# Kernel optimization log

Measured on AMD Instinct MI355X. Metric: run time of the kernel, lower is better.

Reference implementation:

```python
import jax, jax.numpy as jnp
import numpy as np

EPS = 1e-16


def setup_inputs() -> dict:
    key = jax.random.key(0)
    ks = jax.random.split(key, 7)
    B, N, C = 4096, 2048, 128  # batch of heads, memory rows, memory cols
    k = jax.random.normal(ks[0], (B, C), dtype=jnp.float32)
    beta = jax.random.normal(ks[1], (B, 1), dtype=jnp.float32)
    g = jax.random.normal(ks[2], (B, 1), dtype=jnp.float32)
    s = jax.random.normal(ks[3], (B, 3), dtype=jnp.float32)
    gamma = jax.random.normal(ks[4], (B, 1), dtype=jnp.float32)
    w_prev = jax.random.uniform(ks[5], (B, N), dtype=jnp.float32)
    w_prev = w_prev / jnp.sum(w_prev, axis=1, keepdims=True)  # valid weighting
    M = jax.random.normal(ks[6], (N, C), dtype=jnp.float32)  # memory matrix
    return {"k": k, "beta": beta, "g": g, "s": s, "gamma": gamma,
            "w_prev": w_prev, "M": M}


def reference(k, beta, g, s, gamma, w_prev, M):
    # head activations
    beta = jax.nn.softplus(beta)            # [B,1] key strength > 0
    g = jax.nn.sigmoid(g)                   # [B,1] interpolation gate
    s = jax.nn.softmax(s, axis=-1)          # [B,3] shift distribution
    gamma = 1.0 + jax.nn.softplus(gamma)    # [B,1] sharpening >= 1

    # content addressing: cosine similarity k vs memory rows
    k_norm = jnp.linalg.norm(k, axis=-1, keepdims=True)          # [B,1]
    m_norm = jnp.linalg.norm(M, axis=-1, keepdims=True)          # [N,1]
    sim = jnp.einsum('bc,nc->bn', k, M) / (k_norm * m_norm.T + EPS)  # [B,N]
    w_c = jax.nn.softmax(beta * sim, axis=-1)                    # [B,N]

    # interpolation with previous weighting
    w_g = g * w_c + (1.0 - g) * w_prev                           # [B,N]

    # circular convolution with 3-tap shift kernel (shifts -1, 0, +1)
    w_tilde = (s[:, 0:1] * jnp.roll(w_g, 1, axis=1)
               + s[:, 1:2] * w_g
               + s[:, 2:3] * jnp.roll(w_g, -1, axis=1))          # [B,N]

    # sharpening
    w_sharp = w_tilde ** gamma
    w = w_sharp / (jnp.sum(w_sharp, axis=1, keepdims=True) + EPS)
    return w
```

## Files before the change

### kernel.cpp

```cpp
#include <hip/hip_runtime.h>
#include <math.h>

#define NN 2048
#define CC 128
#define EPSF 1e-16f

typedef __attribute__((ext_vector_type(8))) short bf16x8;
typedef __attribute__((ext_vector_type(4))) float f32x4;

__device__ __forceinline__ float softplusf(float x) {
  return fmaxf(x, 0.0f) + log1pf(__expf(-fabsf(x)));
}
__device__ __forceinline__ float wave_sum(float v) {
#pragma unroll
  for (int o = 32; o; o >>= 1) v += __shfl_xor(v, o, 64);
  return v;
}

union U8 { uint u[4]; bf16x8 v; };

__device__ __forceinline__ void split8(float4 a, float4 b, bf16x8& hi,
                                       bf16x8& lo, float& sq) {
  float f[8] = {a.x, a.y, a.z, a.w, b.x, b.y, b.z, b.w};
  U8 H, L;
#pragma unroll
  for (int i = 0; i < 4; ++i) {
    float f0 = f[2 * i], f1 = f[2 * i + 1];
    sq += f0 * f0;
    sq += f1 * f1;
    uint u0 = __float_as_uint(f0), u1 = __float_as_uint(f1);
    uint m0 = u0 & 0xffff0000u, m1 = u1 & 0xffff0000u;
    float r0 = f0 - __uint_as_float(m0);
    float r1 = f1 - __uint_as_float(m1);
    H.u[i] = (u0 >> 16) | m1;
    L.u[i] = (__float_as_uint(r0) >> 16) | (__float_as_uint(r1) & 0xffff0000u);
  }
  hi = H.v;
  lo = L.v;
}

__device__ __forceinline__ void gl2lds16(const void* gsrc, void* ldst) {
  __builtin_amdgcn_global_load_lds(
      (const __attribute__((address_space(1))) void*)gsrc,
      (__attribute__((address_space(3))) void*)ldst, 16, 0, 0);
}

__global__ __launch_bounds__(256) void ntm_prep_kernel(
    const float* __restrict__ kptr, const float* __restrict__ beta_,
    const float* __restrict__ g_, const float* __restrict__ s_,
    const float* __restrict__ gamma_, const float* __restrict__ M,
    bf16x8* __restrict__ Mhf, bf16x8* __restrict__ Mlf,
    bf16x8* __restrict__ Khf, bf16x8* __restrict__ Klf,
    float* __restrict__ imn, float* __restrict__ zb, float* __restrict__ gvv,
    float* __restrict__ gmv, float* __restrict__ s0a, float* __restrict__ s1a,
    float* __restrict__ s2a) {
  const int bid = blockIdx.x;
  const int t = threadIdx.x;
  if (bid < 96) {
    const int lane = t & 63;
    const int wv = t >> 6;
    const int l15 = lane & 15;
    const int lg = lane >> 4;
    const bool isM = bid < 32;
    const int grp = (isM ? bid : bid - 32) * 4 + wv;
    const int nrow = isM ? ((grp >> 3) * 128 + 8 * l15 + (grp & 7))
                         : (grp * 16 + l15);
    const float* src = (isM ? M : kptr) + nrow * CC + lg * 8;
    bf16x8* dh = (isM ? Mhf : Khf) + (grp * 4) * 64 + lane;
    bf16x8* dl = (isM ? Mlf : Klf) + (grp * 4) * 64 + lane;
    float sq = 0.f;
#pragma unroll
    for (int ks = 0; ks < 4; ++ks) {
      float4 a0 = *(const float4*)(src + ks * 32);
      float4 a1 = *(const float4*)(src + ks * 32 + 4);
      bf16x8 h, l;
      split8(a0, a1, h, l, sq);
      dh[ks * 64] = h;
      dl[ks * 64] = l;
    }
    sq += __shfl_xor(sq, 16, 64);
    sq += __shfl_xor(sq, 32, 64);
    if (lg == 0) {
      if (isM) {
        imn[nrow] = 1.0f / sqrtf(sq);
      } else {
        zb[nrow] = softplusf(beta_[nrow]) / sqrtf(sq);
      }
    }
  } else {
    const int r = (bid - 96) * 256 + t;
    gvv[r] = 1.0f / (1.0f + __expf(-g_[r]));
    gmv[r] = 1.0f + softplusf(gamma_[r]);
    float sh0 = s_[3 * r], sh1 = s_[3 * r + 1], sh2 = s_[3 * r + 2];
    float shm = fmaxf(sh0, fmaxf(sh1, sh2));
    float e0 = __expf(sh0 - shm), e1 = __expf(sh1 - shm), e2 = __expf(sh2 - shm);
    float sden = 1.0f / (e0 + e1 + e2);
    s0a[r] = e0 * sden;
    s1a[r] = e1 * sden;
    s2a[r] = e2 * sden;
  }
}

__global__ __launch_bounds__(1024) void ntm_main_kernel(
    const float* __restrict__ w_prev, const bf16x8* __restrict__ Mhf,
    const bf16x8* __restrict__ Mlf, const bf16x8* __restrict__ Khf,
    const bf16x8* __restrict__ Klf, const float* __restrict__ imn,
    const float* __restrict__ zb, const float* __restrict__ gvv,
    const float* __restrict__ gmv, const float* __restrict__ s0a,
    const float* __restrict__ s1a, const float* __restrict__ s2a,
    float* __restrict__ out) {
  __shared__ __align__(16) char smem[131072];
  char* Areg = smem;
  float (*eQ)[2048] = (float(*)[2048])smem;

  const int t = threadIdx.x;
  const int lane = t & 63;
  const int w = __builtin_amdgcn_readfirstlane(t >> 6);
  const int l15 = lane & 15;
  const int lg = lane >> 4;
  const int bg = blockIdx.x;
  const int b0 = bg * 16;

  if (w == 0) {
#pragma unroll
    for (int ks = 0; ks < 4; ++ks) {
      gl2lds16(&Khf[(bg * 4 + ks) * 64 + lane], Areg + (ks * 2 + 0) * 1024);
      gl2lds16(&Klf[(bg * 4 + ks) * 64 + lane], Areg + (ks * 2 + 1) * 1024);
    }
  }
  char* myB = smem + 8192 + w * 4096;
  const int gw = 8 * w;
#define STAGEB(c)                                                          \
  {                                                                        \
    const int ks_ = (c) >> 3, tt_ = (c)&7;                                 \
    gl2lds16(&Mhf[((gw + tt_) * 4 + ks_) * 64 + lane],                     \
             myB + ((c)&1) * 2048);                                        \
    gl2lds16(&Mlf[((gw + tt_) * 4 + ks_) * 64 + lane],                     \
             myB + ((c)&1) * 2048 + 1024);                                 \
  }
  STAGEB(0);
  STAGEB(1);
  __syncthreads();

  f32x4 accT[8];
#pragma unroll
  for (int tt = 0; tt < 8; ++tt) accT[tt] = (f32x4){0.f, 0.f, 0.f, 0.f};

  bf16x8 ah, al;
#pragma unroll
  for (int c = 0; c < 32; ++c) {
    if ((c & 7) == 0) {
      const int ks_ = c >> 3;
      ah = *(const bf16x8*)(Areg + (ks_ * 2 + 0) * 1024 + lane * 16);
      al = *(const bf16x8*)(Areg + (ks_ * 2 + 1) * 1024 + lane * 16);
    }
    if (c == 31) {
      asm volatile("s_waitcnt vmcnt(0)" ::: "memory");
    } else {
      asm volatile("s_waitcnt vmcnt(2)" ::: "memory");
    }
    bf16x8 bh = *(const bf16x8*)(myB + (c & 1) * 2048 + lane * 16);
    bf16x8 bl = *(const bf16x8*)(myB + (c & 1) * 2048 + 1024 + lane * 16);
    asm volatile("s_waitcnt lgkmcnt(0)" ::: "memory");
    if (c + 2 < 32) STAGEB(c + 2);
    const int tt = c & 7;
    accT[tt] = __builtin_amdgcn_mfma_f32_16x16x32_bf16(ah, bh, accT[tt], 0, 0, 0);
    accT[tt] = __builtin_amdgcn_mfma_f32_16x16x32_bf16(al, bh, accT[tt], 0, 0, 0);
    accT[tt] = __builtin_amdgcn_mfma_f32_16x16x32_bf16(ah, bl, accT[tt], 0, 0, 0);
  }
#undef STAGEB

  const int ncol0 = 128 * w + 8 * l15;
  const float4 i0 = *(const float4*)&imn[ncol0];
  const float4 i1 = *(const float4*)&imn[ncol0 + 4];
  float imn_t[8] = {i0.x, i0.y, i0.z, i0.w, i1.x, i1.y, i1.z, i1.w};
#pragma unroll
  for (int q = 0; q < 4; ++q) {
    const float zbv = zb[b0 + lg * 4 + q];
#pragma unroll
    for (int tt = 0; tt < 8; ++tt) {
      accT[tt][q] = __expf(accT[tt][q] * imn_t[tt] * zbv);
    }
  }

  __syncthreads();

#pragma unroll
  for (int q = 0; q < 4; ++q) {
    *(float4*)&eQ[lg * 4 + q][ncol0] =
        (float4){accT[0][q], accT[1][q], accT[2][q], accT[3][q]};
    *(float4*)&eQ[lg * 4 + q][ncol0 + 4] =
        (float4){accT[4][q], accT[5][q], accT[6][q], accT[7][q]};
  }
  __syncthreads();

  float4 v[8];
#pragma unroll
  for (int b = 0; b < 8; ++b)
    v[b] = *(const float4*)&eQ[w][256 * b + 4 * lane];

  const int row = b0 + w;
  const int lanem1 = (lane + 63) & 63;
  const int lanep1 = (lane + 1) & 63;

  float lsum = 0.f;
#pragma unroll
  for (int b = 0; b < 8; ++b)
    lsum += (v[b].x + v[b].y) + (v[b].z + v[b].w);
  const float tot = wave_sum(lsum);

  const float gv = gvv[row];
  const float ge = gv / tot;
  const float om = 1.0f - gv;
  const float sh0 = s0a[row], sh1 = s1a[row], sh2 = s2a[row];
  const float gammav = gmv[row];

  const float4* w_prev4 = (const float4*)w_prev;
  const size_t rf4 = (size_t)row * (NN / 4) + lane;
#pragma unroll
  for (int b = 0; b < 8; ++b) {
    float4 w4 = w_prev4[rf4 + 64 * b];
    v[b].x = ge * v[b].x + om * w4.x;
    v[b].y = ge * v[b].y + om * w4.y;
    v[b].z = ge * v[b].z + om * w4.z;
    v[b].w = ge * v[b].w + om * w4.w;
  }

  float pm[8], np[8];
#pragma unroll
  for (int b = 0; b < 8; ++b) {
    pm[b] = __shfl(v[b].w, lanem1, 64);
    np[b] = __shfl(v[b].x, lanep1, 64);
  }
  float sp = 0.f;
#pragma unroll
  for (int b = 0; b < 8; ++b) {
    const float pv0 = (lane == 0) ? pm[(b + 7) & 7] : pm[b];
    const float nx3 = (lane == 63) ? np[(b + 1) & 7] : np[b];
    const float w0 = v[b].x, w1 = v[b].y, w2 = v[b].z, w3 = v[b].w;
    float t0 = sh0 * pv0 + sh1 * w0 + sh2 * w1;
    float t1 = sh0 * w0 + sh1 * w1 + sh2 * w2;
    float t2 = sh0 * w1 + sh1 * w2 + sh2 * w3;
    float t3 = sh0 * w2 + sh1 * w3 + sh2 * nx3;
    float p0 = __expf(gammav * __logf(t0));
    float p1 = __expf(gammav * __logf(t1));
    float p2 = __expf(gammav * __logf(t2));
    float p3 = __expf(gammav * __logf(t3));
    v[b].x = p0;
    v[b].y = p1;
    v[b].z = p2;
    v[b].w = p3;
    sp += (p0 + p1) + (p2 + p3);
  }
  const float spt = wave_sum(sp);
  const float pinv = 1.0f / (spt + EPSF);

  float4* out4 = (float4*)out;
#pragma unroll
  for (int b = 0; b < 8; ++b) {
    float4 o;
    o.x = v[b].x * pinv;
    o.y = v[b].y * pinv;
    o.z = v[b].z * pinv;
    o.w = v[b].w * pinv;
    out4[rf4 + 64 * b] = o;
  }
}

__global__ __launch_bounds__(1024) void ntm_main_fallback(
    const float* __restrict__ kptr, const float* __restrict__ beta_,
    const float* __restrict__ g_, const float* __restrict__ s_,
    const float* __restrict__ gamma_, const float* __restrict__ w_prev,
    const float* __restrict__ Mptr, float* __restrict__ out) {
  __shared__ float red[16][16];
  __shared__ float edges[16][16][2];
  const int t = threadIdx.x;
  const int lane = t & 63;
  const int w = __builtin_amdgcn_readfirstlane(t >> 6);
  const int l15 = lane & 15;
  const int lg = lane >> 4;
  const int b0 = blockIdx.x * 16;

  const float* kr = kptr + (b0 + l15) * CC + lg * 8;
  bf16x8 ah[4], al[4];
  float ksq = 0.f;
#pragma unroll
  for (int ks = 0; ks < 4; ++ks) {
    float4 a0 = *(const float4*)(kr + ks * 32);
    float4 a1 = *(const float4*)(kr + ks * 32 + 4);
    split8(a0, a1, ah[ks], al[ks], ksq);
  }
  ksq += __shfl_xor(ksq, 16, 64);
  ksq += __shfl_xor(ksq, 32, 64);
  const float ikn_own = 1.0f / sqrtf(ksq);

  f32x4 accT[8];
  float imn[8];
#pragma unroll
  for (int tt = 0; tt < 8; ++tt) {
    const int n0t = 128 * w + 16 * tt;
    const float* mr = Mptr + (size_t)(n0t + l15) * CC + lg * 8;
    f32x4 acc = {0.f, 0.f, 0.f, 0.f};
    float msq = 0.f;
#pragma unroll
    for (int ks = 0; ks < 4; ++ks) {
      float4 m0 = *(const float4*)(mr + ks * 32);
      float4 m1 = *(const float4*)(mr + ks * 32 + 4);
      bf16x8 bh, bl;
      split8(m0, m1, bh, bl, msq);
      acc = __builtin_amdgcn_mfma_f32_16x16x32_bf16(ah[ks], bh, acc, 0, 0, 0);
      acc = __builtin_amdgcn_mfma_f32_16x16x32_bf16(al[ks], bh, acc, 0, 0, 0);
      acc = __builtin_amdgcn_mfma_f32_16x16x32_bf16(ah[ks], bl, acc, 0, 0, 0);
    }
    msq += __shfl_xor(msq, 16, 64);
    msq += __shfl_xor(msq, 32, 64);
    imn[tt] = 1.0f / sqrtf(msq);
    accT[tt] = acc;
  }

#pragma unroll
  for (int q = 0; q < 4; ++q) {
    const int rr = lg * 4 + q;
    const float zb = softplusf(beta_[b0 + rr]) * __shfl(ikn_own, rr, 64);
    float rs = 0.f;
#pragma unroll
    for (int tt = 0; tt < 8; ++tt) {
      float e = __expf(accT[tt][q] * imn[tt] * zb);
      accT[tt][q] = e;
      rs += e;
    }
    rs += __shfl_xor(rs, 1, 64);
    rs += __shfl_xor(rs, 2, 64);
    rs += __shfl_xor(rs, 4, 64);
    rs += __shfl_xor(rs, 8, 64);
    if (l15 == 0) red[rr][w] = rs;
  }
  __syncthreads();

#pragma unroll
  for (int q = 0; q < 4; ++q) {
    const int rr = lg * 4 + q;
    float4 p0 = *(const float4*)&red[rr][0];
    float4 p1 = *(const float4*)&red[rr][4];
    float4 p2 = *(const float4*)&red[rr][8];
    float4 p3 = *(const float4*)&red[rr][12];
    float tot = (p0.x + p0.y + p0.z + p0.w) + (p1.x + p1.y + p1.z + p1.w) +
                (p2.x + p2.y + p2.z + p2.w) + (p3.x + p3.y + p3.z + p3.w);
    const float gv = 1.0f / (1.0f + __expf(-g_[b0 + rr]));
    const float ge = gv / tot;
    const float om = 1.0f - gv;
    const size_t rbase = (size_t)(b0 + rr) * NN + 128 * w + l15;
#pragma unroll
    for (int tt = 0; tt < 8; ++tt) {
      float wpv = w_prev[rbase + 16 * tt];
      accT[tt][q] = ge * accT[tt][q] + om * wpv;
    }
    if (l15 == 0) edges[rr][w][0] = accT[0][q];
    if (l15 == 15) edges[rr][w][1] = accT[7][q];
  }
  __syncthreads();

  const int tm = (lane & 48) | ((lane + 15) & 15);
  const int tp = (lane & 48) | ((lane + 1) & 15);
#pragma unroll
  for (int q = 0; q < 4; ++q) {
    const int rr = lg * 4 + q;
    float sh0 = s_[3 * (b0 + rr)];
    float sh1 = s_[3 * (b0 + rr) + 1];
    float sh2 = s_[3 * (b0 + rr) + 2];
    float shm = fmaxf(sh0, fmaxf(sh1, sh2));
    float e0 = __expf(sh0 - shm), e1 = __expf(sh1 - shm), e2 = __expf(sh2 - shm);
    float sden = 1.0f / (e0 + e1 + e2);
    sh0 = e0 * sden; sh1 = e1 * sden; sh2 = e2 * sden;
    const float gammav = 1.0f + softplusf(gamma_[b0 + rr]);
    const float eL = edges[rr][(w + 15) & 15][1];
    const float eR = edges[rr][(w + 1) & 15][0];
    float sm[8], sp[8];
#pragma unroll
    for (int tt = 0; tt < 8; ++tt) {
      sm[tt] = __shfl(accT[tt][q], tm, 64);
      sp[tt] = __shfl(accT[tt][q], tp, 64);
    }
    float rs = 0.f;
#pragma unroll
    for (int tt = 0; tt < 8; ++tt) {
      float pv = (l15 == 0) ? ((tt == 0) ? eL : sm[tt - 1]) : sm[tt];
      float nx = (l15 == 15) ? ((tt == 7) ? eR : sp[tt + 1]) : sp[tt];
      float wt = sh0 * pv + sh1 * accT[tt][q] + sh2 * nx;
      float p = __expf(gammav * __logf(wt));
      accT[tt][q] = p;
      rs += p;
    }
    rs += __shfl_xor(rs, 1, 64);
    rs += __shfl_xor(rs, 2, 64);
    rs += __shfl_xor(rs, 4, 64);
    rs += __shfl_xor(rs, 8, 64);
    if (l15 == 0) red[rr][w] = rs;
  }
  __syncthreads();

#pragma unroll
  for (int q = 0; q < 4; ++q) {
    const int rr = lg * 4 + q;
    float4 p0 = *(const float4*)&red[rr][0];
    float4 p1 = *(const float4*)&red[rr][4];
    float4 p2 = *(const float4*)&red[rr][8];
    float4 p3 = *(const float4*)&red[rr][12];
    float tot = (p0.x + p0.y + p0.z + p0.w) + (p1.x + p1.y + p1.z + p1.w) +
                (p2.x + p2.y + p2.z + p2.w) + (p3.x + p3.y + p3.z + p3.w);
    const float pinv = 1.0f / (tot + EPSF);
    const size_t rbase = (size_t)(b0 + rr) * NN + 128 * w + l15;
#pragma unroll
    for (int tt = 0; tt < 8; ++tt) {
      out[rbase + 16 * tt] = accT[tt][q] * pinv;
    }
  }
}

extern "C" void kernel_launch(void* const* d_in, const int* in_sizes, int n_in,
                              void* d_out, int out_size, void* d_ws, size_t ws_size,
                              hipStream_t stream) {
  const float* k = (const float*)d_in[0];
  const float* beta = (const float*)d_in[1];
  const float* g = (const float*)d_in[2];
  const float* s = (const float*)d_in[3];
  const float* gamma = (const float*)d_in[4];
  const float* w_prev = (const float*)d_in[5];
  const float* M = (const float*)d_in[6];
  float* out = (float*)d_out;

  char* ws = (char*)d_ws;
  bf16x8* Mhf = (bf16x8*)(ws + 0);
  bf16x8* Mlf = (bf16x8*)(ws + 524288);
  bf16x8* Khf = (bf16x8*)(ws + 1048576);
  bf16x8* Klf = (bf16x8*)(ws + 2097152);
  float* imn = (float*)(ws + 3145728);
  float* zb = imn + 2048;
  float* gvv = zb + 4096;
  float* gmv = gvv + 4096;
  float* s0a = gmv + 4096;
  float* s1a = s0a + 4096;
  float* s2a = s1a + 4096;
  const size_t need = 3145728 + 2048 * 4 + 6 * 4096 * 4;

  if (ws_size >= need) {
    ntm_prep_kernel<<<112, 256, 0, stream>>>(k, beta, g, s, gamma, M, Mhf, Mlf,
                                             Khf, Klf, imn, zb, gvv, gmv, s0a,
                                             s1a, s2a);
    ntm_main_kernel<<<256, 1024, 0, stream>>>(w_prev, Mhf, Mlf, Khf, Klf, imn,
                                              zb, gvv, gmv, s0a, s1a, s2a, out);
  } else {
    ntm_main_fallback<<<256, 1024, 0, stream>>>(k, beta, g, s, gamma, w_prev,
                                                M, out);
  }
}
```

Measured before the change: 39.25 us.

## Prescale M and k by norms in prep, triple-buffer M tiles, raise MFMA priority

```diff
diff --git a/kernel.cpp b/kernel.cpp
--- a/kernel.cpp
+++ b/kernel.cpp
@@ -19,15 +19,11 @@
 
 union U8 { uint u[4]; bf16x8 v; };
 
-__device__ __forceinline__ void split8(float4 a, float4 b, bf16x8& hi,
-                                       bf16x8& lo, float& sq) {
-  float f[8] = {a.x, a.y, a.z, a.w, b.x, b.y, b.z, b.w};
+__device__ __forceinline__ void split8s(const float* f, bf16x8& hi, bf16x8& lo) {
   U8 H, L;
 #pragma unroll
   for (int i = 0; i < 4; ++i) {
     float f0 = f[2 * i], f1 = f[2 * i + 1];
-    sq += f0 * f0;
-    sq += f1 * f1;
     uint u0 = __float_as_uint(f0), u1 = __float_as_uint(f1);
     uint m0 = u0 & 0xffff0000u, m1 = u1 & 0xffff0000u;
     float r0 = f0 - __uint_as_float(m0);
@@ -51,8 +47,8 @@
     const float* __restrict__ gamma_, const float* __restrict__ M,
     bf16x8* __restrict__ Mhf, bf16x8* __restrict__ Mlf,
     bf16x8* __restrict__ Khf, bf16x8* __restrict__ Klf,
-    float* __restrict__ imn, float* __restrict__ zb, float* __restrict__ gvv,
-    float* __restrict__ gmv, float* __restrict__ s0a, float* __restrict__ s1a,
+    float* __restrict__ gvv, float* __restrict__ gmv,
+    float* __restrict__ s0a, float* __restrict__ s1a,
     float* __restrict__ s2a) {
   const int bid = blockIdx.x;
   const int t = threadIdx.x;
@@ -68,24 +64,30 @@
     const float* src = (isM ? M : kptr) + nrow * CC + lg * 8;
     bf16x8* dh = (isM ? Mhf : Khf) + (grp * 4) * 64 + lane;
     bf16x8* dl = (isM ? Mlf : Klf) + (grp * 4) * 64 + lane;
+
+    float f[4][8];
     float sq = 0.f;
 #pragma unroll
     for (int ks = 0; ks < 4; ++ks) {
       float4 a0 = *(const float4*)(src + ks * 32);
       float4 a1 = *(const float4*)(src + ks * 32 + 4);
+      f[ks][0] = a0.x; f[ks][1] = a0.y; f[ks][2] = a0.z; f[ks][3] = a0.w;
+      f[ks][4] = a1.x; f[ks][5] = a1.y; f[ks][6] = a1.z; f[ks][7] = a1.w;
+#pragma unroll
+      for (int j = 0; j < 8; ++j) sq += f[ks][j] * f[ks][j];
+    }
+    sq += __shfl_xor(sq, 16, 64);
+    sq += __shfl_xor(sq, 32, 64);
+    const float nrm = sqrtf(sq);
+    const float scale = isM ? (1.0f / nrm) : (softplusf(beta_[nrow]) / nrm);
+#pragma unroll
+    for (int ks = 0; ks < 4; ++ks) {
+#pragma unroll
+      for (int j = 0; j < 8; ++j) f[ks][j] *= scale;
       bf16x8 h, l;
-      split8(a0, a1, h, l, sq);
+      split8s(f[ks], h, l);
       dh[ks * 64] = h;
       dl[ks * 64] = l;
-    }
-    sq += __shfl_xor(sq, 16, 64);
-    sq += __shfl_xor(sq, 32, 64);
-    if (lg == 0) {
-      if (isM) {
-        imn[nrow] = 1.0f / sqrtf(sq);
-      } else {
-        zb[nrow] = softplusf(beta_[nrow]) / sqrtf(sq);
-      }
     }
   } else {
     const int r = (bid - 96) * 256 + t;
@@ -104,8 +106,7 @@
 __global__ __launch_bounds__(1024) void ntm_main_kernel(
     const float* __restrict__ w_prev, const bf16x8* __restrict__ Mhf,
     const bf16x8* __restrict__ Mlf, const bf16x8* __restrict__ Khf,
-    const bf16x8* __restrict__ Klf, const float* __restrict__ imn,
-    const float* __restrict__ zb, const float* __restrict__ gvv,
+    const bf16x8* __restrict__ Klf, const float* __restrict__ gvv,
     const float* __restrict__ gmv, const float* __restrict__ s0a,
     const float* __restrict__ s1a, const float* __restrict__ s2a,
     float* __restrict__ out) {
@@ -128,18 +129,19 @@
       gl2lds16(&Klf[(bg * 4 + ks) * 64 + lane], Areg + (ks * 2 + 1) * 1024);
     }
   }
-  char* myB = smem + 8192 + w * 4096;
+  char* myB = smem + 8192 + w * 6144;
   const int gw = 8 * w;
 #define STAGEB(c)                                                          \
   {                                                                        \
     const int ks_ = (c) >> 3, tt_ = (c)&7;                                 \
     gl2lds16(&Mhf[((gw + tt_) * 4 + ks_) * 64 + lane],                     \
-             myB + ((c)&1) * 2048);                                        \
+             myB + ((c) % 3) * 2048);                                      \
     gl2lds16(&Mlf[((gw + tt_) * 4 + ks_) * 64 + lane],                     \
-             myB + ((c)&1) * 2048 + 1024);                                 \
+             myB + ((c) % 3) * 2048 + 1024);                               \
   }
   STAGEB(0);
   STAGEB(1);
+  STAGEB(2);
   __syncthreads();
 
   f32x4 accT[8];
@@ -154,32 +156,32 @@
       ah = *(const bf16x8*)(Areg + (ks_ * 2 + 0) * 1024 + lane * 16);
       al = *(const bf16x8*)(Areg + (ks_ * 2 + 1) * 1024 + lane * 16);
     }
-    if (c == 31) {
+    if (c <= 29) {
+      asm volatile("s_waitcnt vmcnt(4)" ::: "memory");
+    } else if (c == 30) {
+      asm volatile("s_waitcnt vmcnt(2)" ::: "memory");
+    } else {
       asm volatile("s_waitcnt vmcnt(0)" ::: "memory");
-    } else {
-      asm volatile("s_waitcnt vmcnt(2)" ::: "memory");
-    }
-    bf16x8 bh = *(const bf16x8*)(myB + (c & 1) * 2048 + lane * 16);
-    bf16x8 bl = *(const bf16x8*)(myB + (c & 1) * 2048 + 1024 + lane * 16);
+    }
+    bf16x8 bh = *(const bf16x8*)(myB + (c % 3) * 2048 + lane * 16);
+    bf16x8 bl = *(const bf16x8*)(myB + (c % 3) * 2048 + 1024 + lane * 16);
     asm volatile("s_waitcnt lgkmcnt(0)" ::: "memory");
-    if (c + 2 < 32) STAGEB(c + 2);
+    if (c + 3 < 32) STAGEB(c + 3);
     const int tt = c & 7;
+    __builtin_amdgcn_s_setprio(1);
     accT[tt] = __builtin_amdgcn_mfma_f32_16x16x32_bf16(ah, bh, accT[tt], 0, 0, 0);
     accT[tt] = __builtin_amdgcn_mfma_f32_16x16x32_bf16(al, bh, accT[tt], 0, 0, 0);
     accT[tt] = __builtin_amdgcn_mfma_f32_16x16x32_bf16(ah, bl, accT[tt], 0, 0, 0);
+    __builtin_amdgcn_s_setprio(0);
   }
 #undef STAGEB
 
   const int ncol0 = 128 * w + 8 * l15;
-  const float4 i0 = *(const float4*)&imn[ncol0];
-  const float4 i1 = *(const float4*)&imn[ncol0 + 4];
-  float imn_t[8] = {i0.x, i0.y, i0.z, i0.w, i1.x, i1.y, i1.z, i1.w};
-#pragma unroll
-  for (int q = 0; q < 4; ++q) {
-    const float zbv = zb[b0 + lg * 4 + q];
-#pragma unroll
-    for (int tt = 0; tt < 8; ++tt) {
-      accT[tt][q] = __expf(accT[tt][q] * imn_t[tt] * zbv);
+#pragma unroll
+  for (int q = 0; q < 4; ++q) {
+#pragma unroll
+    for (int tt = 0; tt < 8; ++tt) {
+      accT[tt][q] = __expf(accT[tt][q]);
     }
   }
 
@@ -267,6 +269,27 @@
   }
 }
 
+union U8F { uint u[4]; bf16x8 v; };
+__device__ __forceinline__ void split8f(float4 a, float4 b, bf16x8& hi,
+                                        bf16x8& lo, float& sq) {
+  float f[8] = {a.x, a.y, a.z, a.w, b.x, b.y, b.z, b.w};
+  U8F H, L;
+#pragma unroll
+  for (int i = 0; i < 4; ++i) {
+    float f0 = f[2 * i], f1 = f[2 * i + 1];
+    sq += f0 * f0;
+    sq += f1 * f1;
+    uint u0 = __float_as_uint(f0), u1 = __float_as_uint(f1);
+    uint m0 = u0 & 0xffff0000u, m1 = u1 & 0xffff0000u;
+    float r0 = f0 - __uint_as_float(m0);
+    float r1 = f1 - __uint_as_float(m1);
+    H.u[i] = (u0 >> 16) | m1;
+    L.u[i] = (__float_as_uint(r0) >> 16) | (__float_as_uint(r1) & 0xffff0000u);
+  }
+  hi = H.v;
+  lo = L.v;
+}
+
 __global__ __launch_bounds__(1024) void ntm_main_fallback(
     const float* __restrict__ kptr, const float* __restrict__ beta_,
     const float* __restrict__ g_, const float* __restrict__ s_,
@@ -288,7 +311,7 @@
   for (int ks = 0; ks < 4; ++ks) {
     float4 a0 = *(const float4*)(kr + ks * 32);
     float4 a1 = *(const float4*)(kr + ks * 32 + 4);
-    split8(a0, a1, ah[ks], al[ks], ksq);
+    split8f(a0, a1, ah[ks], al[ks], ksq);
   }
   ksq += __shfl_xor(ksq, 16, 64);
   ksq += __shfl_xor(ksq, 32, 64);
@@ -307,7 +330,7 @@
       float4 m0 = *(const float4*)(mr + ks * 32);
       float4 m1 = *(const float4*)(mr + ks * 32 + 4);
       bf16x8 bh, bl;
-      split8(m0, m1, bh, bl, msq);
+      split8f(m0, m1, bh, bl, msq);
       acc = __builtin_amdgcn_mfma_f32_16x16x32_bf16(ah[ks], bh, acc, 0, 0, 0);
       acc = __builtin_amdgcn_mfma_f32_16x16x32_bf16(al[ks], bh, acc, 0, 0, 0);
       acc = __builtin_amdgcn_mfma_f32_16x16x32_bf16(ah[ks], bl, acc, 0, 0, 0);
@@ -434,21 +457,18 @@
   bf16x8* Mlf = (bf16x8*)(ws + 524288);
   bf16x8* Khf = (bf16x8*)(ws + 1048576);
   bf16x8* Klf = (bf16x8*)(ws + 2097152);
-  float* imn = (float*)(ws + 3145728);
-  float* zb = imn + 2048;
-  float* gvv = zb + 4096;
+  float* gvv = (float*)(ws + 3145728);
   float* gmv = gvv + 4096;
   float* s0a = gmv + 4096;
   float* s1a = s0a + 4096;
   float* s2a = s1a + 4096;
-  const size_t need = 3145728 + 2048 * 4 + 6 * 4096 * 4;
+  const size_t need = 3145728 + 5 * 4096 * 4;
 
   if (ws_size >= need) {
     ntm_prep_kernel<<<112, 256, 0, stream>>>(k, beta, g, s, gamma, M, Mhf, Mlf,
-                                             Khf, Klf, imn, zb, gvv, gmv, s0a,
-                                             s1a, s2a);
-    ntm_main_kernel<<<256, 1024, 0, stream>>>(w_prev, Mhf, Mlf, Khf, Klf, imn,
-                                              zb, gvv, gmv, s0a, s1a, s2a, out);
+                                             Khf, Klf, gvv, gmv, s0a, s1a, s2a);
+    ntm_main_kernel<<<256, 1024, 0, stream>>>(w_prev, Mhf, Mlf, Khf, Klf, gvv,
+                                              gmv, s0a, s1a, s2a, out);
   } else {
     ntm_main_fallback<<<256, 1024, 0, stream>>>(k, beta, g, s, gamma, w_prev,
                                                 M, out);
```

Measured after the change: 40.17 us. +2.3%, slower.
